# Kernel optimization log

Hardware: AMD Instinct MI355X
Metric: run time of the kernel (lower is better)

Reference implementation:

```python
import jax, jax.numpy as jnp
import numpy as np

B, S, N_IN, N_OUT = 4, 192, 256, 1

def setup_inputs() -> dict:
    key = jax.random.key(0)
    ks = jax.random.split(key, 7)
    scale = 1.0 / np.sqrt(N_IN)
    return {
        "h_head": jax.random.normal(ks[0], (B, S, N_IN), jnp.float32),
        "h_dep": jax.random.normal(ks[1], (B, S, N_IN), jnp.float32),
        "h_sib": jax.random.normal(ks[2], (B, S, N_IN), jnp.float32),
        "W_tri": jax.random.normal(ks[3], (N_OUT, N_IN, N_IN, N_IN), jnp.float32) * (scale / N_IN),
        "U_hd": jax.random.normal(ks[4], (N_OUT, N_IN, N_IN), jnp.float32) * scale,
        "V_hs": jax.random.normal(ks[5], (N_OUT, N_IN, N_IN), jnp.float32) * scale,
        "Z_ds": jax.random.normal(ks[6], (N_OUT, N_IN, N_IN), jnp.float32) * scale,
        "bias": jnp.zeros((N_OUT,), jnp.float32),
    }

def reference(h_head, h_dep, h_sib, W_tri, U_hd, V_hs, Z_ds, bias):
    # biaffine terms: [b, x, y, o]
    s_hd = jnp.einsum('bhi,oij,bdj->bhdo', h_head, U_hd, h_dep)
    s_hs = jnp.einsum('bhi,oij,bsj->bhso', h_head, V_hs, h_sib)
    s_ds = jnp.einsum('bdi,oij,bsj->bdso', h_dep, Z_ds, h_sib)
    # trilinear term: note j,k of W_tri appear nowhere else, so they are
    # reduced first (w_red[o,i] = sum_{j,k} W_tri[o,i,j,k]) — same math as
    # torch.einsum('bhi,bdi,bsi,oijk->bhdso', ...).
    w_red = jnp.sum(W_tri, axis=(2, 3))  # [o, i]
    s_tri = jnp.einsum('bhi,bdi,bsi,oi->bhdso', h_head, h_dep, h_sib, w_red)
    scores = (s_tri
              + s_hd[:, :, :, None, :]   # unsqueeze sib axis
              + s_hs[:, :, None, :, :]   # unsqueeze dep axis
              + s_ds[:, None, :, :, :]   # unsqueeze head axis
              + bias)
    return scores[..., 0]  # n_out == 1 -> squeeze last dim
```

## Files before the change

kernel.cpp:

```cpp
#include <hip/hip_runtime.h>
#include <stdint.h>

#define NB 4
#define SS 192
#define NI 256

typedef __attribute__((ext_vector_type(8))) short bf16x8;
typedef __attribute__((ext_vector_type(16))) float f32x16;

__device__ __forceinline__ uint16_t f2bf(float f) {
  union { float f; uint32_t u; } v; v.f = f;
  return (uint16_t)((v.u + 0x7FFFu + ((v.u >> 16) & 1u)) >> 16);
}

__device__ __forceinline__ uint4 pack8(const float4 a, const float4 b) {
  uint4 r;
  r.x = (uint32_t)f2bf(a.x) | ((uint32_t)f2bf(a.y) << 16);
  r.y = (uint32_t)f2bf(a.z) | ((uint32_t)f2bf(a.w) << 16);
  r.z = (uint32_t)f2bf(b.x) | ((uint32_t)f2bf(b.y) << 16);
  r.w = (uint32_t)f2bf(b.z) | ((uint32_t)f2bf(b.w) << 16);
  return r;
}

__device__ __forceinline__ uint32_t bfmul2(uint32_t x, uint32_t y) {
  union { float f; uint32_t u; } xa, xb, ya, yb, r0, r1;
  xa.u = x << 16;        ya.u = y << 16;
  xb.u = x & 0xFFFF0000u; yb.u = y & 0xFFFF0000u;
  r0.f = xa.f * ya.f;
  r1.f = xb.f * yb.f;
  uint32_t lo = (r0.u + 0x7FFFu + ((r0.u >> 16) & 1u)) >> 16;
  uint32_t hi = (r1.u + 0x7FFFu + ((r1.u >> 16) & 1u)) >> 16;
  return lo | (hi << 16);
}


__global__ __launch_bounds__(512) void kA(
    const float* __restrict__ W,
    const float* __restrict__ h_head, const float* __restrict__ h_dep, const float* __restrict__ h_sib,
    const float* __restrict__ U, const float* __restrict__ V, const float* __restrict__ Z,
    float* __restrict__ partial,
    uint16_t* __restrict__ HH, uint16_t* __restrict__ HS,
    float* __restrict__ s_hd, float* __restrict__ s_hs, float* __restrict__ s_ds) {
  const int bi = blockIdx.x, tid = threadIdx.x;

  if (bi >= 60) {
    __shared__ float red[8];
    const int c = bi - 60;
    const float4* pw = (const float4*)(W + (size_t)c * 16384);
    float4 a = {0.f, 0.f, 0.f, 0.f};
    #pragma unroll
    for (int it = 0; it < 8; ++it) {
      const float4 v = pw[it * 512 + tid];
      a.x += v.x; a.y += v.y; a.z += v.z; a.w += v.w;
    }
    float s = (a.x + a.y) + (a.z + a.w);
    for (int off = 32; off > 0; off >>= 1) s += __shfl_down(s, off, 64);
    if ((tid & 63) == 0) red[tid >> 6] = s;
    __syncthreads();
    if (tid == 0) {
      float t = 0.f;
      #pragma unroll
      for (int q = 0; q < 8; ++q) t += red[q];
      partial[c] = t;
    }
    return;
  }
  if (bi >= 12) {
    const int rl = tid >> 5, c8 = tid & 31;
    const int g = (bi - 12) * 16 + rl;
    const int dst = g * 32 + (c8 ^ (g & 15));
    const int srci = g * 64 + c8 * 2;
    { const float4 x = ((const float4*)h_head)[srci], y = ((const float4*)h_head)[srci + 1];
      ((uint4*)HH)[dst] = pack8(x, y); }
    { const float4 x = ((const float4*)h_sib)[srci], y = ((const float4*)h_sib)[srci + 1];
      ((uint4*)HS)[dst] = pack8(x, y); }
    return;
  }

  __shared__ __align__(16) unsigned char smem[147456];
  unsigned char* Ah1 = smem;
  unsigned char* Bh1 = smem + 49152;
  unsigned char* Qb  = smem;
  unsigned char* Ah2 = smem + 98304;
  const int which = bi >> 2, b = bi & 3;
  const float* A1 = (which == 0) ? h_dep : h_sib;
  const float* B1 = (which == 0) ? U : (which == 1) ? V : Z;
  const float* A2 = (which == 2) ? h_dep : h_head;
  float* Os = (which == 0) ? s_hd : (which == 1) ? s_hs : s_ds;
  const int lane = tid & 63, w = tid >> 6;
  const int l31 = lane & 31, l5 = lane >> 5;

  f32x16 acc1[6] = {};
  #pragma unroll
  for (int kh = 0; kh < 2; ++kh) {
    const int kbase = kh * 128;
    if (kh) __syncthreads();
    #pragma unroll
    for (int i = 0; i < 6; ++i) {
      const int slot = i * 512 + tid;
      const int row = slot >> 4, ck = slot & 15;
      const float* sp = A1 + (size_t)(b * SS + row) * NI + kbase + ck * 8;
      const float4 x = *(const float4*)sp, y = *(const float4*)(sp + 4);
      *(uint4*)(Ah1 + row * 256 + ((ck ^ (row & 15)) << 4)) = pack8(x, y);
    }
    #pragma unroll
    for (int i = 0; i < 8; ++i) {
      const int slot = i * 512 + tid;
      const int row = slot >> 4, ck = slot & 15;
      const float* sp = B1 + (size_t)row * NI + kbase + ck * 8;
      const float4 x = *(const float4*)sp, y = *(const float4*)(sp + 4);
      *(uint4*)(Bh1 + row * 256 + ((ck ^ (row & 15)) << 4)) = pack8(x, y);
    }
    __syncthreads();
    const int brow = w * 32 + l31;
    const int bbyte = brow * 256;
    const int bmask = brow & 15;
    #pragma unroll
    for (int ks = 0; ks < 8; ++ks) {
      const int sl = ks * 2 + l5;
      bf16x8 bf = *reinterpret_cast<const bf16x8*>(Bh1 + bbyte + ((sl ^ bmask) << 4));
      #pragma unroll
      for (int mt = 0; mt < 6; ++mt) {
        const int ar = mt * 32 + l31;
        bf16x8 af = *reinterpret_cast<const bf16x8*>(Ah1 + ar * 256 + ((sl ^ (ar & 15)) << 4));
        acc1[mt] = __builtin_amdgcn_mfma_f32_32x32x16_bf16(af, bf, acc1[mt], 0, 0, 0);
      }
    }
  }
  __syncthreads();

  {
    const int i = w * 32 + l31;
    unsigned char* Qh = Qb + (w >> 2) * 49152;
    const int ic = i & 127, ck = ic >> 3, pos = i & 7;
    #pragma unroll
    for (int mt = 0; mt < 6; ++mt) {
      #pragma unroll
      for (int r = 0; r < 16; ++r) {
        const int m = mt * 32 + (r & 3) + 8 * (r >> 2) + 4 * l5;
        *(uint16_t*)(Qh + m * 256 + ((ck ^ (m & 15)) << 4) + pos * 2) = f2bf(acc1[mt][r]);
      }
    }
  }
  __syncthreads();

  f32x16 acc2[6] = {};
  #pragma unroll
  for (int kh = 0; kh < 2; ++kh) {
    const int kbase = kh * 128;
    if (kh) __syncthreads();
    #pragma unroll
    for (int i = 0; i < 6; ++i) {
      const int slot = i * 512 + tid;
      const int row = slot >> 4, ck = slot & 15;
      const float* sp = A2 + (size_t)(b * SS + row) * NI + kbase + ck * 8;
      const float4 x = *(const float4*)sp, y = *(const float4*)(sp + 4);
      *(uint4*)(Ah2 + row * 256 + ((ck ^ (row & 15)) << 4)) = pack8(x, y);
    }
    __syncthreads();
    if (w < 6) {
      const unsigned char* Qh = Qb + kh * 49152;
      const int brow = w * 32 + l31;
      const int bbyte = brow * 256;
      const int bmask = brow & 15;
      #pragma unroll
      for (int ks = 0; ks < 8; ++ks) {
        const int sl = ks * 2 + l5;
        bf16x8 bf = *reinterpret_cast<const bf16x8*>(Qh + bbyte + ((sl ^ bmask) << 4));
        #pragma unroll
        for (int mt = 0; mt < 6; ++mt) {
          const int ar = mt * 32 + l31;
          bf16x8 af = *reinterpret_cast<const bf16x8*>(Ah2 + ar * 256 + ((sl ^ (ar & 15)) << 4));
          acc2[mt] = __builtin_amdgcn_mfma_f32_32x32x16_bf16(af, bf, acc2[mt], 0, 0, 0);
        }
      }
    }
  }
  if (w < 6) {
    const int n = w * 32 + l31;
    #pragma unroll
    for (int mt = 0; mt < 6; ++mt) {
      #pragma unroll
      for (int r = 0; r < 16; ++r) {
        const int m = mt * 32 + (r & 3) + 8 * (r >> 2) + 4 * l5;
        Os[(size_t)(b * SS + m) * SS + n] = acc2[mt][r];
      }
    }
  }
}

__global__ __launch_bounds__(576) void k3_big(
    const uint16_t* __restrict__ HH, const uint16_t* __restrict__ HS,
    const float* __restrict__ h_dep, const float* __restrict__ partial,
    const float* __restrict__ s_hd, const float* __restrict__ s_hs,
    const float* __restrict__ s_ds,
    const float* __restrict__ bias, float* __restrict__ out) {
  __shared__ __align__(16) uint16_t Btile[96 * 128];
  __shared__ __align__(16) uint16_t Atile[96 * 128];
  __shared__ uint16_t cvec[NI];
  __shared__ float chd_s[96];
  const int d = blockIdx.x, hb = blockIdx.y >> 1, sb = blockIdx.y & 1, b = blockIdx.z;
  const int tid = threadIdx.x;
  const int lane = tid & 63, w = tid >> 6;
  const int wh = w / 3, ws = w % 3;
  const int l31 = lane & 31, l5 = lane >> 5;

  if (tid < NI) {
    const float wr = partial[4 * tid] + partial[4 * tid + 1]
                   + partial[4 * tid + 2] + partial[4 * tid + 3];
    cvec[tid] = f2bf(wr * h_dep[(b * SS + d) * NI + tid]);
  } else if (tid < NI + 96) {
    const int t = tid - NI;
    chd_s[t] = s_hd[(size_t)(b * SS + hb * 96 + t) * SS + d];
  }
  __syncthreads();

  f32x16 acc = {};

  #pragma unroll
  for (int half = 0; half < 2; ++half) {
    const int kbase = half * 128;
    if (half) __syncthreads();
    #pragma unroll
    for (int i = 0; i < 3; ++i) {
      const int slot = i * 576 + tid;
      if (slot < 1536) {
        const int row = slot >> 4;
        const uint16_t* src = HS + ((size_t)(b * SS + sb * 96 + row) << 8) + kbase + (slot & 15) * 8;
        __builtin_amdgcn_global_load_lds(
            (const __attribute__((address_space(1))) void*)src,
            (__attribute__((address_space(3))) void*)(Btile + (size_t)slot * 8),
            16, 0, 0);
      }
    }
    #pragma unroll
    for (int i = 0; i < 3; ++i) {
      const int slot = i * 576 + tid;
      if (slot < 1536) {
        const int row = slot >> 4;
        const int kc = slot & 15;
        const int lcl = kc ^ (row & 15);
        const uint4 cv4 = *(const uint4*)(cvec + kbase + lcl * 8);
        const uint4 hh4 = *(const uint4*)(HH + ((size_t)(b * SS + hb * 96 + row) << 8) + kbase + kc * 8);
        uint4 a4;
        a4.x = bfmul2(hh4.x, cv4.x);
        a4.y = bfmul2(hh4.y, cv4.y);
        a4.z = bfmul2(hh4.z, cv4.z);
        a4.w = bfmul2(hh4.w, cv4.w);
        *(uint4*)((char*)Atile + (size_t)slot * 16) = a4;
      }
    }
    __syncthreads();
    const int arow = wh * 32 + l31;
    const int abyte = arow * 256;
    const int amask = arow & 15;
    const int brow = ws * 32 + l31;
    const int bbyte = brow * 256;
    const int bmask = brow & 15;
    #pragma unroll
    for (int ks = 0; ks < 8; ++ks) {
      const int sl = ks * 2 + l5;
      bf16x8 af = *reinterpret_cast<const bf16x8*>((const char*)Atile + abyte + ((sl ^ amask) << 4));
      bf16x8 bf = *reinterpret_cast<const bf16x8*>((const char*)Btile + bbyte + ((sl ^ bmask) << 4));
      acc = __builtin_amdgcn_mfma_f32_32x32x16_bf16(af, bf, acc, 0, 0, 0);
    }
  }

  const float bias0 = bias[0];
  const int s = sb * 96 + ws * 32 + l31;
  const float dsv = s_ds[(b * SS + d) * SS + s];
  #pragma unroll
  for (int r = 0; r < 16; ++r) {
    const int hl = wh * 32 + (r & 3) + 8 * (r >> 2) + 4 * l5;
    const float v = acc[r] + chd_s[hl] + bias0
                  + s_hs[(size_t)(b * SS + hb * 96 + hl) * SS + s] + dsv;
    out[((size_t)(b * SS + hb * 96 + hl) * SS + d) * SS + s] = v;
  }
}

extern "C" void kernel_launch(void* const* d_in, const int* in_sizes, int n_in,
                              void* d_out, int out_size, void* d_ws, size_t ws_size,
                              hipStream_t stream) {
  const float* h_head = (const float*)d_in[0];
  const float* h_dep  = (const float*)d_in[1];
  const float* h_sib  = (const float*)d_in[2];
  const float* W_tri  = (const float*)d_in[3];
  const float* U_hd   = (const float*)d_in[4];
  const float* V_hs   = (const float*)d_in[5];
  const float* Z_ds   = (const float*)d_in[6];
  const float* bias   = (const float*)d_in[7];
  float* out = (float*)d_out;

  float* ws = (float*)d_ws;
  float* partial = ws;          ws += 1024;
  float* s_hd    = ws;          ws += NB * SS * SS;
  float* s_hs    = ws;          ws += NB * SS * SS;
  float* s_ds    = ws;          ws += NB * SS * SS;
  uint16_t* HH   = (uint16_t*)ws;
  uint16_t* HS   = HH + NB * SS * NI;

  kA<<<1084, 512, 0, stream>>>(W_tri, h_head, h_dep, h_sib, U_hd, V_hs, Z_ds,
                               partial, HH, HS, s_hd, s_hs, s_ds);
  k3_big<<<dim3(SS, 4, NB), 576, 0, stream>>>(HH, HS, h_dep, partial,
                                              s_hd, s_hs, s_ds, bias, out);
}
```

Baseline: 73.54 us.

## Switch bf16 path to fp16 with hardware converts and transpose s_hd storage

Replaces the software bf16 rounding (integer add/shift sequences) with hardware fp16 packed conversion (cvt_pkrtz) and packed half multiply, and uses fp16 MFMA instead of bf16 MFMA. For the head-dep biaffine term it swaps the MFMA operand roles so the result is stored transposed, which lets k3_big read its 96 chd values contiguously instead of with stride SS. The aim is fewer ALU instructions in the packing and scaling loops and a coalesced load. The cost is fp16's narrower range, which could overflow or lose precision on intermediate products.

```diff
diff --git a/kernel.cpp b/kernel.cpp
--- a/kernel.cpp
+++ b/kernel.cpp
@@ -1,36 +1,39 @@
 #include <hip/hip_runtime.h>
+#include <hip/hip_fp16.h>
 #include <stdint.h>
 
 #define NB 4
 #define SS 192
 #define NI 256
 
-typedef __attribute__((ext_vector_type(8))) short bf16x8;
+typedef __attribute__((ext_vector_type(8))) _Float16 f16x8;
+typedef __attribute__((ext_vector_type(2))) __fp16 fp16v2;
 typedef __attribute__((ext_vector_type(16))) float f32x16;
 
-__device__ __forceinline__ uint16_t f2bf(float f) {
-  union { float f; uint32_t u; } v; v.f = f;
-  return (uint16_t)((v.u + 0x7FFFu + ((v.u >> 16) & 1u)) >> 16);
-}
-
-__device__ __forceinline__ uint4 pack8(const float4 a, const float4 b) {
+__device__ __forceinline__ uint16_t f2h(float f) {
+  union { _Float16 h; uint16_t u; } t; t.h = (_Float16)f; return t.u;
+}
+
+__device__ __forceinline__ uint32_t cvt2(float lo, float hi) {
+  union { fp16v2 h; uint32_t u; } t;
+  t.h = __builtin_amdgcn_cvt_pkrtz(lo, hi);
+  return t.u;
+}
+
+__device__ __forceinline__ uint4 pack8h(const float4 a, const float4 b) {
   uint4 r;
-  r.x = (uint32_t)f2bf(a.x) | ((uint32_t)f2bf(a.y) << 16);
-  r.y = (uint32_t)f2bf(a.z) | ((uint32_t)f2bf(a.w) << 16);
-  r.z = (uint32_t)f2bf(b.x) | ((uint32_t)f2bf(b.y) << 16);
-  r.w = (uint32_t)f2bf(b.z) | ((uint32_t)f2bf(b.w) << 16);
+  r.x = cvt2(a.x, a.y);
+  r.y = cvt2(a.z, a.w);
+  r.z = cvt2(b.x, b.y);
+  r.w = cvt2(b.z, b.w);
   return r;
 }
 
-__device__ __forceinline__ uint32_t bfmul2(uint32_t x, uint32_t y) {
-  union { float f; uint32_t u; } xa, xb, ya, yb, r0, r1;
-  xa.u = x << 16;        ya.u = y << 16;
-  xb.u = x & 0xFFFF0000u; yb.u = y & 0xFFFF0000u;
-  r0.f = xa.f * ya.f;
-  r1.f = xb.f * yb.f;
-  uint32_t lo = (r0.u + 0x7FFFu + ((r0.u >> 16) & 1u)) >> 16;
-  uint32_t hi = (r1.u + 0x7FFFu + ((r1.u >> 16) & 1u)) >> 16;
-  return lo | (hi << 16);
+__device__ __forceinline__ uint32_t hmul2(uint32_t x, uint32_t y) {
+  union { uint32_t u; __half2 h; } a, b, c;
+  a.u = x; b.u = y;
+  c.h = __hmul2(a.h, b.h);
+  return c.u;
 }
 
 
@@ -40,7 +43,7 @@
     const float* __restrict__ U, const float* __restrict__ V, const float* __restrict__ Z,
     float* __restrict__ partial,
     uint16_t* __restrict__ HH, uint16_t* __restrict__ HS,
-    float* __restrict__ s_hd, float* __restrict__ s_hs, float* __restrict__ s_ds) {
+    float* __restrict__ s_hdT, float* __restrict__ s_hs, float* __restrict__ s_ds) {
   const int bi = blockIdx.x, tid = threadIdx.x;
 
   if (bi >= 60) {
@@ -71,9 +74,9 @@
     const int dst = g * 32 + (c8 ^ (g & 15));
     const int srci = g * 64 + c8 * 2;
     { const float4 x = ((const float4*)h_head)[srci], y = ((const float4*)h_head)[srci + 1];
-      ((uint4*)HH)[dst] = pack8(x, y); }
+      ((uint4*)HH)[dst] = pack8h(x, y); }
     { const float4 x = ((const float4*)h_sib)[srci], y = ((const float4*)h_sib)[srci + 1];
-      ((uint4*)HS)[dst] = pack8(x, y); }
+      ((uint4*)HS)[dst] = pack8h(x, y); }
     return;
   }
 
@@ -86,7 +89,7 @@
   const float* A1 = (which == 0) ? h_dep : h_sib;
   const float* B1 = (which == 0) ? U : (which == 1) ? V : Z;
   const float* A2 = (which == 2) ? h_dep : h_head;
-  float* Os = (which == 0) ? s_hd : (which == 1) ? s_hs : s_ds;
+  float* Os = (which == 0) ? s_hdT : (which == 1) ? s_hs : s_ds;
   const int lane = tid & 63, w = tid >> 6;
   const int l31 = lane & 31, l5 = lane >> 5;
 
@@ -101,7 +104,7 @@
       const int row = slot >> 4, ck = slot & 15;
       const float* sp = A1 + (size_t)(b * SS + row) * NI + kbase + ck * 8;
       const float4 x = *(const float4*)sp, y = *(const float4*)(sp + 4);
-      *(uint4*)(Ah1 + row * 256 + ((ck ^ (row & 15)) << 4)) = pack8(x, y);
+      *(uint4*)(Ah1 + row * 256 + ((ck ^ (row & 15)) << 4)) = pack8h(x, y);
     }
     #pragma unroll
     for (int i = 0; i < 8; ++i) {
@@ -109,7 +112,7 @@
       const int row = slot >> 4, ck = slot & 15;
       const float* sp = B1 + (size_t)row * NI + kbase + ck * 8;
       const float4 x = *(const float4*)sp, y = *(const float4*)(sp + 4);
-      *(uint4*)(Bh1 + row * 256 + ((ck ^ (row & 15)) << 4)) = pack8(x, y);
+      *(uint4*)(Bh1 + row * 256 + ((ck ^ (row & 15)) << 4)) = pack8h(x, y);
     }
     __syncthreads();
     const int brow = w * 32 + l31;
@@ -118,12 +121,12 @@
     #pragma unroll
     for (int ks = 0; ks < 8; ++ks) {
       const int sl = ks * 2 + l5;
-      bf16x8 bf = *reinterpret_cast<const bf16x8*>(Bh1 + bbyte + ((sl ^ bmask) << 4));
+      f16x8 bf = *reinterpret_cast<const f16x8*>(Bh1 + bbyte + ((sl ^ bmask) << 4));
       #pragma unroll
       for (int mt = 0; mt < 6; ++mt) {
         const int ar = mt * 32 + l31;
-        bf16x8 af = *reinterpret_cast<const bf16x8*>(Ah1 + ar * 256 + ((sl ^ (ar & 15)) << 4));
-        acc1[mt] = __builtin_amdgcn_mfma_f32_32x32x16_bf16(af, bf, acc1[mt], 0, 0, 0);
+        f16x8 af = *reinterpret_cast<const f16x8*>(Ah1 + ar * 256 + ((sl ^ (ar & 15)) << 4));
+        acc1[mt] = __builtin_amdgcn_mfma_f32_32x32x16_f16(af, bf, acc1[mt], 0, 0, 0);
       }
     }
   }
@@ -138,7 +141,7 @@
       #pragma unroll
       for (int r = 0; r < 16; ++r) {
         const int m = mt * 32 + (r & 3) + 8 * (r >> 2) + 4 * l5;
-        *(uint16_t*)(Qh + m * 256 + ((ck ^ (m & 15)) << 4) + pos * 2) = f2bf(acc1[mt][r]);
+        *(uint16_t*)(Qh + m * 256 + ((ck ^ (m & 15)) << 4) + pos * 2) = f2h(acc1[mt][r]);
       }
     }
   }
@@ -155,23 +158,23 @@
       const int row = slot >> 4, ck = slot & 15;
       const float* sp = A2 + (size_t)(b * SS + row) * NI + kbase + ck * 8;
       const float4 x = *(const float4*)sp, y = *(const float4*)(sp + 4);
-      *(uint4*)(Ah2 + row * 256 + ((ck ^ (row & 15)) << 4)) = pack8(x, y);
+      *(uint4*)(Ah2 + row * 256 + ((ck ^ (row & 15)) << 4)) = pack8h(x, y);
     }
     __syncthreads();
     if (w < 6) {
       const unsigned char* Qh = Qb + kh * 49152;
       const int brow = w * 32 + l31;
-      const int bbyte = brow * 256;
-      const int bmask = brow & 15;
       #pragma unroll
       for (int ks = 0; ks < 8; ++ks) {
         const int sl = ks * 2 + l5;
-        bf16x8 bf = *reinterpret_cast<const bf16x8*>(Qh + bbyte + ((sl ^ bmask) << 4));
+        const unsigned char* mTile = (which == 0) ? Qh : Ah2;
+        const unsigned char* nTile = (which == 0) ? Ah2 : Qh;
+        f16x8 bf = *reinterpret_cast<const f16x8*>(nTile + brow * 256 + ((sl ^ (brow & 15)) << 4));
         #pragma unroll
         for (int mt = 0; mt < 6; ++mt) {
           const int ar = mt * 32 + l31;
-          bf16x8 af = *reinterpret_cast<const bf16x8*>(Ah2 + ar * 256 + ((sl ^ (ar & 15)) << 4));
-          acc2[mt] = __builtin_amdgcn_mfma_f32_32x32x16_bf16(af, bf, acc2[mt], 0, 0, 0);
+          f16x8 af = *reinterpret_cast<const f16x8*>(mTile + ar * 256 + ((sl ^ (ar & 15)) << 4));
+          acc2[mt] = __builtin_amdgcn_mfma_f32_32x32x16_f16(af, bf, acc2[mt], 0, 0, 0);
         }
       }
     }
@@ -192,12 +195,12 @@
 __global__ __launch_bounds__(576) void k3_big(
     const uint16_t* __restrict__ HH, const uint16_t* __restrict__ HS,
     const float* __restrict__ h_dep, const float* __restrict__ partial,
-    const float* __restrict__ s_hd, const float* __restrict__ s_hs,
+    const float* __restrict__ s_hdT, const float* __restrict__ s_hs,
     const float* __restrict__ s_ds,
     const float* __restrict__ bias, float* __restrict__ out) {
   __shared__ __align__(16) uint16_t Btile[96 * 128];
   __shared__ __align__(16) uint16_t Atile[96 * 128];
-  __shared__ uint16_t cvec[NI];
+  __shared__ __align__(16) uint16_t cvec[NI];
   __shared__ float chd_s[96];
   const int d = blockIdx.x, hb = blockIdx.y >> 1, sb = blockIdx.y & 1, b = blockIdx.z;
   const int tid = threadIdx.x;
@@ -208,10 +211,10 @@
   if (tid < NI) {
     const float wr = partial[4 * tid] + partial[4 * tid + 1]
                    + partial[4 * tid + 2] + partial[4 * tid + 3];
-    cvec[tid] = f2bf(wr * h_dep[(b * SS + d) * NI + tid]);
+    cvec[tid] = f2h(wr * h_dep[(size_t)(b * SS + d) * NI + tid]);
   } else if (tid < NI + 96) {
     const int t = tid - NI;
-    chd_s[t] = s_hd[(size_t)(b * SS + hb * 96 + t) * SS + d];
+    chd_s[t] = s_hdT[(size_t)(b * SS + d) * SS + hb * 96 + t];
   }
   __syncthreads();
 
@@ -243,10 +246,10 @@
         const uint4 cv4 = *(const uint4*)(cvec + kbase + lcl * 8);
         const uint4 hh4 = *(const uint4*)(HH + ((size_t)(b * SS + hb * 96 + row) << 8) + kbase + kc * 8);
         uint4 a4;
-        a4.x = bfmul2(hh4.x, cv4.x);
-        a4.y = bfmul2(hh4.y, cv4.y);
-        a4.z = bfmul2(hh4.z, cv4.z);
-        a4.w = bfmul2(hh4.w, cv4.w);
+        a4.x = hmul2(hh4.x, cv4.x);
+        a4.y = hmul2(hh4.y, cv4.y);
+        a4.z = hmul2(hh4.z, cv4.z);
+        a4.w = hmul2(hh4.w, cv4.w);
         *(uint4*)((char*)Atile + (size_t)slot * 16) = a4;
       }
     }
@@ -260,15 +263,15 @@
     #pragma unroll
     for (int ks = 0; ks < 8; ++ks) {
       const int sl = ks * 2 + l5;
-      bf16x8 af = *reinterpret_cast<const bf16x8*>((const char*)Atile + abyte + ((sl ^ amask) << 4));
-      bf16x8 bf = *reinterpret_cast<const bf16x8*>((const char*)Btile + bbyte + ((sl ^ bmask) << 4));
-      acc = __builtin_amdgcn_mfma_f32_32x32x16_bf16(af, bf, acc, 0, 0, 0);
+      f16x8 af = *reinterpret_cast<const f16x8*>((const char*)Atile + abyte + ((sl ^ amask) << 4));
+      f16x8 bf = *reinterpret_cast<const f16x8*>((const char*)Btile + bbyte + ((sl ^ bmask) << 4));
+      acc = __builtin_amdgcn_mfma_f32_32x32x16_f16(af, bf, acc, 0, 0, 0);
     }
   }
 
   const float bias0 = bias[0];
   const int s = sb * 96 + ws * 32 + l31;
-  const float dsv = s_ds[(b * SS + d) * SS + s];
+  const float dsv = s_ds[(size_t)(b * SS + d) * SS + s];
   #pragma unroll
   for (int r = 0; r < 16; ++r) {
     const int hl = wh * 32 + (r & 3) + 8 * (r >> 2) + 4 * l5;
@@ -293,14 +296,14 @@
 
   float* ws = (float*)d_ws;
   float* partial = ws;          ws += 1024;
-  float* s_hd    = ws;          ws += NB * SS * SS;
+  float* s_hdT   = ws;          ws += NB * SS * SS;
   float* s_hs    = ws;          ws += NB * SS * SS;
   float* s_ds    = ws;          ws += NB * SS * SS;
   uint16_t* HH   = (uint16_t*)ws;
   uint16_t* HS   = HH + NB * SS * NI;
 
   kA<<<1084, 512, 0, stream>>>(W_tri, h_head, h_dep, h_sib, U_hd, V_hs, Z_ds,
-                               partial, HH, HS, s_hd, s_hs, s_ds);
+                               partial, HH, HS, s_hdT, s_hs, s_ds);
   k3_big<<<dim3(SS, 4, NB), 576, 0, stream>>>(HH, HS, h_dep, partial,
-                                              s_hd, s_hs, s_ds, bias, out);
-}
+                                              s_hdT, s_hs, s_ds, bias, out);
+}
```

Result: faster. 66.72 us (-9.3%).
